# Optimization experiments

Hardware: AMD Instinct MI355X
Metric: run time of the kernel (lower is better)

The kernel has to match this reference:

```python
import jax, jax.numpy as jnp
import numpy as np

D_MODEL = 1024
NUM_HEADS = 16
D_K = D_MODEL // NUM_HEADS


def setup_inputs() -> dict:
    key = jax.random.key(0)
    ks = jax.random.split(key, 11)
    B, S = 2, 2048
    scale = 1.0 / np.sqrt(D_MODEL)
    inp = {
        'q': jax.random.normal(ks[0], (B, S, D_MODEL), jnp.float32),
        'k': jax.random.normal(ks[1], (B, S, D_MODEL), jnp.float32),
        'v': jax.random.normal(ks[2], (B, S, D_MODEL), jnp.float32),
        'Wq': jax.random.normal(ks[3], (D_MODEL, D_MODEL), jnp.float32) * scale,
        'bq': jnp.zeros((D_MODEL,), jnp.float32),
        'Wk': jax.random.normal(ks[4], (D_MODEL, D_MODEL), jnp.float32) * scale,
        'bk': jnp.zeros((D_MODEL,), jnp.float32),
        'Wv': jax.random.normal(ks[5], (D_MODEL, D_MODEL), jnp.float32) * scale,
        'bv': jnp.zeros((D_MODEL,), jnp.float32),
        'Wo': jax.random.normal(ks[6], (D_MODEL, D_MODEL), jnp.float32) * scale,
        'bo': jnp.zeros((D_MODEL,), jnp.float32),
    }
    return inp


def _split_heads(x):
    # [B, S, d_model] -> [B, H, S, d_k]
    B, S, _ = x.shape
    return x.reshape(B, S, NUM_HEADS, D_K).transpose(0, 2, 1, 3)


def reference(q, k, v, Wq, bq, Wk, bk, Wv, bv, Wo, bo):
    B, S, _ = q.shape
    qh = _split_heads(q @ Wq + bq)
    kh = _split_heads(k @ Wk + bk)
    vh = _split_heads(v @ Wv + bv)
    scores = jnp.einsum('bhsd,bhtd->bhst', qh, kh) / np.sqrt(D_K)
    attn = jax.nn.softmax(scores, axis=-1)  # dropout is identity in eval
    out = jnp.einsum('bhst,bhtd->bhsd', attn, vh)
    out = out.transpose(0, 2, 1, 3).reshape(B, S, D_MODEL)
    return out @ Wo + bo
```

## Files before the change

kernel.cpp:

```cpp
#include <hip/hip_runtime.h>

typedef unsigned short u16;
typedef unsigned int u32;
typedef __attribute__((ext_vector_type(4))) float f32x4;
typedef __attribute__((ext_vector_type(16))) float f32x16;
typedef __attribute__((ext_vector_type(8))) short bf16x8;
typedef __attribute__((ext_vector_type(4))) unsigned short u16x4;
typedef __attribute__((ext_vector_type(8))) unsigned short u16x8;
typedef __attribute__((ext_vector_type(4))) unsigned int u32x4;

#define S_LEN 2048
#define DMODEL 1024

__device__ __forceinline__ float bf2f(u16 u) {
  union { unsigned int i; float f; } c; c.i = ((unsigned int)u) << 16; return c.f;
}
__device__ __forceinline__ u16 f2bf(float f) {
  union { float f; unsigned int i; } c; c.f = f;
  unsigned int v = c.i + 0x7FFFu + ((c.i >> 16) & 1u);
  return (u16)(v >> 16);
}
__device__ __forceinline__ u32 cvtpk(float lo, float hi) {
  u32 r;
  asm("v_cvt_pk_bf16_f32 %0, %1, %2" : "=v"(r) : "v"(lo), "v"(hi));
  return r;
}

typedef const __attribute__((address_space(1))) void gv_t;
typedef __attribute__((address_space(3))) void lv_t;
__device__ __forceinline__ void gload_lds16(const void* g, void* l) {
  __builtin_amdgcn_global_load_lds((gv_t*)g, (lv_t*)l, 16, 0, 0);
}

__global__ __launch_bounds__(256) void k_cvt(const float* __restrict__ src,
                                             u16* __restrict__ dst, int n8) {
  int i = blockIdx.x * 256 + threadIdx.x;
  if (i >= n8) return;
  f32x4 a = ((const f32x4*)src)[i * 2];
  f32x4 b = ((const f32x4*)src)[i * 2 + 1];
  u16x8 o;
#pragma unroll
  for (int j = 0; j < 4; ++j) { o[j] = f2bf(a[j]); o[j + 4] = f2bf(b[j]); }
  ((u16x8*)dst)[i] = o;
}

__global__ __launch_bounds__(256) void k_twcvt(const float* __restrict__ src,
                                               u16* __restrict__ dst, int R, int C) {
  __shared__ u16 tile[64][68];
  int tiles_c = C >> 6;
  int tr = blockIdx.x / tiles_c, tc = blockIdx.x - tr * tiles_c;
  int r0 = tr << 6, c0 = tc << 6;
  int t = threadIdx.x;
#pragma unroll
  for (int i = 0; i < 4; ++i) {
    int e = (t + i * 256) << 2;
    int rr = e >> 6, cc = e & 63;
    f32x4 v = *(const f32x4*)&src[(size_t)(r0 + rr) * C + (c0 + cc)];
#pragma unroll
    for (int j = 0; j < 4; ++j) tile[rr][cc + j] = f2bf(v[j]);
  }
  __syncthreads();
#pragma unroll
  for (int i = 0; i < 4; ++i) {
    int e = (t + i * 256) << 2;
    int rr = e >> 6, cc = e & 63;
    u16x4 v;
#pragma unroll
    for (int j = 0; j < 4; ++j) v[j] = tile[cc + j][rr];
    *(u16x4*)&dst[(size_t)(c0 + rr) * R + (r0 + cc)] = v;
  }
}

__global__ __launch_bounds__(256) void k_packK(const u16* __restrict__ Ck,
                                               u16* __restrict__ Kp) {
  int flat = blockIdx.x * 256 + threadIdx.x;
  int lane = flat & 63, kd = (flat >> 6) & 3, kt = (flat >> 8) & 63;
  int h = (flat >> 14) & 15, b = flat >> 18;
  int l31 = lane & 31, hi = lane >> 5;
  const u16* src = &Ck[(size_t)(b * 2048 + kt * 32 + l31) * 1024 + h * 64 + kd * 16 + hi * 8];
  ((u16x8*)Kp)[flat] = *(const u16x8*)src;
}

__global__ __launch_bounds__(256) void k_packV(const u16* __restrict__ Cv,
                                               u16* __restrict__ Vp) {
  int flat = blockIdx.x * 256 + threadIdx.x;
  int lane = flat & 63, ks = (flat >> 6) & 3, dvh = (flat >> 8) & 1;
  int kt = (flat >> 9) & 31, h = (flat >> 14) & 15, b = flat >> 18;
  int l31 = lane & 31, hi = lane >> 5;
  const u16* src = &Cv[(size_t)(b * 2048 + kt * 64 + ks * 16 + hi * 8) * 1024 + h * 64 + dvh * 32 + l31];
  u16x8 o;
#pragma unroll
  for (int j = 0; j < 8; ++j) o[j] = src[(size_t)j * 1024];
  ((u16x8*)Vp)[flat] = o;
}

struct GemmSet { const u16* A; const u16* Bt; const float* bias; void* C; };
struct GemmArgs { GemmSet s[3]; };

template <int OUTF32>
__global__ __launch_bounds__(256) void k_gemm_bt(GemmArgs ga) {
  constexpr int K = 1024, N = 1024;
  __shared__ __align__(16) u16 Al[128 * 32];
  __shared__ __align__(16) u16 Bl[128 * 32];
  int mat = blockIdx.x >> 8;
  int t = blockIdx.x & 255;
  int m0 = (t & 31) << 7;
  int n0 = (t >> 5) << 7;
  const u16* A = ga.s[mat].A;
  const u16* Bt = ga.s[mat].Bt;
  int lane = threadIdx.x & 63, w = threadIdx.x >> 6;
  int g = lane >> 4, cl = lane & 15;
  int wr = w >> 1, wc = w & 1;
  f32x4 zero4 = {0.f, 0.f, 0.f, 0.f};
  f32x4 acc[4][4];
#pragma unroll
  for (int i = 0; i < 4; ++i)
#pragma unroll
    for (int j = 0; j < 4; ++j) acc[i][j] = zero4;

  int srow0 = w * 32 + (lane >> 2);
  int scol = (lane & 3) << 3;
  for (int kt = 0; kt < K / 32; ++kt) {
    int k0 = kt << 5;
#pragma unroll
    for (int c = 0; c < 2; ++c) {
      int row = srow0 + c * 16;
      gload_lds16(&A[(size_t)(m0 + row) * K + k0 + scol], &Al[w * 1024 + c * 512]);
      gload_lds16(&Bt[(size_t)(n0 + row) * K + k0 + scol], &Bl[w * 1024 + c * 512]);
    }
    __syncthreads();
    bf16x8 af[4], bfm[4];
#pragma unroll
    for (int i = 0; i < 4; ++i) {
      af[i]  = *(const bf16x8*)&Al[(wr * 64 + i * 16 + cl) * 32 + g * 8];
      bfm[i] = *(const bf16x8*)&Bl[(wc * 64 + i * 16 + cl) * 32 + g * 8];
    }
#pragma unroll
    for (int mi = 0; mi < 4; ++mi)
#pragma unroll
      for (int ni = 0; ni < 4; ++ni)
        acc[mi][ni] = __builtin_amdgcn_mfma_f32_16x16x32_bf16(af[mi], bfm[ni], acc[mi][ni], 0, 0, 0);
    __syncthreads();
  }
  const float* bias = ga.s[mat].bias;
#pragma unroll
  for (int ni = 0; ni < 4; ++ni) {
    int n = n0 + wc * 64 + ni * 16 + cl;
    float bv = bias[n];
#pragma unroll
    for (int mi = 0; mi < 4; ++mi) {
      int r0 = m0 + wr * 64 + mi * 16 + g * 4;
#pragma unroll
      for (int r = 0; r < 4; ++r) {
        float val = acc[mi][ni][r] + bv;
        if (OUTF32) ((float*)ga.s[mat].C)[(size_t)(r0 + r) * N + n] = val;
        else        ((u16*)ga.s[mat].C)[(size_t)(r0 + r) * N + n] = f2bf(val);
      }
    }
  }
}

__global__ __launch_bounds__(256) void k_attn2(const u16* __restrict__ Q,
                                               const u16* __restrict__ Kp,
                                               const u16* __restrict__ Vp,
                                               u16* __restrict__ O) {
  int lane = threadIdx.x & 63, w = threadIdx.x >> 6;
  int l31 = lane & 31, hi = lane >> 5;
  int bx = blockIdx.x;
  int logical = (bx & 7) * 64 + (bx >> 3);
  int bh = logical >> 4, qt = logical & 15;
  int b = bh >> 4, h = bh & 15;
  const u16* Qb = Q + (size_t)b * S_LEN * DMODEL + h * 64;
  const u16* Kph = Kp + (size_t)(b * 16 + h) * (64 * 4 * 64 * 8);
  const u16* Vph = Vp + (size_t)(b * 16 + h) * (32 * 2 * 4 * 64 * 8);
  u16* Ob = O + (size_t)b * S_LEN * DMODEL + h * 64;
  int qbase = qt * 128 + w * 32;

  bf16x8 qf[4];
  const u16* qp = &Qb[(size_t)(qbase + l31) * DMODEL + hi * 8];
#pragma unroll
  for (int kd = 0; kd < 4; ++kd) qf[kd] = *(const bf16x8*)&qp[kd * 16];

  f32x16 zero16 = {0};
  f32x16 oa0 = zero16, oa1 = zero16;
  float m = -3.0e38f, lsum = 0.f;
  const float INVSQ = 0.125f;

  for (int kt = 0; kt < S_LEN / 64; ++kt) {
    const u16* kpt = Kph + (size_t)kt * 4096 + (size_t)lane * 8;
    const u16* vpt = Vph + (size_t)kt * 4096 + (size_t)lane * 8;
    bf16x8 vf0[4], vf1[4];
#pragma unroll
    for (int ks = 0; ks < 4; ++ks) {
      vf0[ks] = *(const bf16x8*)&vpt[ks * 512];
      vf1[ks] = *(const bf16x8*)&vpt[2048 + ks * 512];
    }
    f32x16 s0 = zero16, s1 = zero16;
#pragma unroll
    for (int kd = 0; kd < 4; ++kd) {
      bf16x8 kfa = *(const bf16x8*)&kpt[kd * 512];
      bf16x8 kfb = *(const bf16x8*)&kpt[2048 + kd * 512];
      s0 = __builtin_amdgcn_mfma_f32_32x32x16_bf16(kfa, qf[kd], s0, 0, 0, 0);
      s1 = __builtin_amdgcn_mfma_f32_32x32x16_bf16(kfb, qf[kd], s1, 0, 0, 0);
    }

    float t0 = fmaxf(s0[0], s0[1]), t1 = fmaxf(s0[2], s0[3]);
    float t2 = fmaxf(s0[4], s0[5]), t3 = fmaxf(s0[6], s0[7]);
#pragma unroll
    for (int r = 8; r < 16; r += 4) {
      t0 = fmaxf(t0, fmaxf(s0[r], s0[r + 1]));
      t1 = fmaxf(t1, fmaxf(s0[r + 2], s0[r + 3]));
    }
#pragma unroll
    for (int r = 0; r < 16; r += 4) {
      t2 = fmaxf(t2, fmaxf(s1[r], s1[r + 1]));
      t3 = fmaxf(t3, fmaxf(s1[r + 2], s1[r + 3]));
    }
    float tm = fmaxf(fmaxf(t0, t1), fmaxf(t2, t3));

    if (!__all(tm <= m + 64.0f)) {
      float tmf = fmaxf(tm, __shfl_xor(tm, 32, 64));
      float mnew = fmaxf(m, tmf);
      float alpha = __expf((m - mnew) * INVSQ);
#pragma unroll
      for (int r = 0; r < 16; ++r) {
        float ar = __shfl(alpha, ((r & 3) + 8 * (r >> 2)) + 4 * hi, 64);
        oa0[r] *= ar; oa1[r] *= ar;
      }
      lsum *= alpha;
      m = mnew;
    }

    float rs0 = 0.f, rs1 = 0.f;
#pragma unroll
    for (int r = 0; r < 16; ++r) {
      float p0 = __expf((s0[r] - m) * INVSQ);
      float p1 = __expf((s1[r] - m) * INVSQ);
      s0[r] = p0; s1[r] = p1;
      rs0 += p0; rs1 += p1;
    }
    float rs = rs0 + rs1;
    lsum += rs + __shfl_xor(rs, 32, 64);

    bf16x8 af[4];
    {
      u32 w0 = cvtpk(s0[0], s0[1]),  w1 = cvtpk(s0[2], s0[3]);
      u32 w2 = cvtpk(s0[4], s0[5]),  w3 = cvtpk(s0[6], s0[7]);
      u32 w4 = cvtpk(s0[8], s0[9]),  w5 = cvtpk(s0[10], s0[11]);
      u32 w6 = cvtpk(s0[12], s0[13]), w7 = cvtpk(s0[14], s0[15]);
      u32 x0 = __shfl_xor(w0, 32, 64), x1 = __shfl_xor(w1, 32, 64);
      u32 x2 = __shfl_xor(w2, 32, 64), x3 = __shfl_xor(w3, 32, 64);
      u32 x4 = __shfl_xor(w4, 32, 64), x5 = __shfl_xor(w5, 32, 64);
      u32 x6 = __shfl_xor(w6, 32, 64), x7 = __shfl_xor(w7, 32, 64);
      union { u32x4 u; bf16x8 v; } c0, c1;
      c0.u = u32x4{hi ? x2 : w0, hi ? x3 : w1, hi ? w2 : x0, hi ? w3 : x1};
      c1.u = u32x4{hi ? x6 : w4, hi ? x7 : w5, hi ? w6 : x4, hi ? w7 : x5};
      af[0] = c0.v; af[1] = c1.v;
    }
    {
      u32 w0 = cvtpk(s1[0], s1[1]),  w1 = cvtpk(s1[2], s1[3]);
      u32 w2 = cvtpk(s1[4], s1[5]),  w3 = cvtpk(s1[6], s1[7]);
      u32 w4 = cvtpk(s1[8], s1[9]),  w5 = cvtpk(s1[10], s1[11]);
      u32 w6 = cvtpk(s1[12], s1[13]), w7 = cvtpk(s1[14], s1[15]);
      u32 x0 = __shfl_xor(w0, 32, 64), x1 = __shfl_xor(w1, 32, 64);
      u32 x2 = __shfl_xor(w2, 32, 64), x3 = __shfl_xor(w3, 32, 64);
      u32 x4 = __shfl_xor(w4, 32, 64), x5 = __shfl_xor(w5, 32, 64);
      u32 x6 = __shfl_xor(w6, 32, 64), x7 = __shfl_xor(w7, 32, 64);
      union { u32x4 u; bf16x8 v; } c0, c1;
      c0.u = u32x4{hi ? x2 : w0, hi ? x3 : w1, hi ? w2 : x0, hi ? w3 : x1};
      c1.u = u32x4{hi ? x6 : w4, hi ? x7 : w5, hi ? w6 : x4, hi ? w7 : x5};
      af[2] = c0.v; af[3] = c1.v;
    }

#pragma unroll
    for (int ks = 0; ks < 4; ++ks) {
      oa0 = __builtin_amdgcn_mfma_f32_32x32x16_bf16(af[ks], vf0[ks], oa0, 0, 0, 0);
      oa1 = __builtin_amdgcn_mfma_f32_32x32x16_bf16(af[ks], vf1[ks], oa1, 0, 0, 0);
    }
  }

  float invl = 1.0f / lsum;
#pragma unroll
  for (int r = 0; r < 16; ++r) {
    float ir = __shfl(invl, ((r & 3) + 8 * (r >> 2)) + 4 * hi, 64);
    int row = qbase + ((r & 3) + 8 * (r >> 2)) + 4 * hi;
    Ob[(size_t)row * DMODEL + l31]      = f2bf(oa0[r] * ir);
    Ob[(size_t)row * DMODEL + 32 + l31] = f2bf(oa1[r] * ir);
  }
}

extern "C" void kernel_launch(void* const* d_in, const int* in_sizes, int n_in,
                              void* d_out, int out_size, void* d_ws, size_t ws_size,
                              hipStream_t stream) {
  const float* q  = (const float*)d_in[0];
  const float* k  = (const float*)d_in[1];
  const float* v  = (const float*)d_in[2];
  const float* Wq = (const float*)d_in[3];
  const float* bq = (const float*)d_in[4];
  const float* Wk = (const float*)d_in[5];
  const float* bk = (const float*)d_in[6];
  const float* Wv = (const float*)d_in[7];
  const float* bv = (const float*)d_in[8];
  const float* Wo = (const float*)d_in[9];
  const float* bo = (const float*)d_in[10];
  float* out = (float*)d_out;
  char* ws = (char*)d_ws;
  const size_t MB = 1024 * 1024;
  u16* wtq = (u16*)(ws + 0 * MB);
  u16* wtk = (u16*)(ws + 2 * MB);
  u16* wtv = (u16*)(ws + 4 * MB);
  u16* wto = (u16*)(ws + 6 * MB);
  u16* qb  = (u16*)(ws + 8 * MB);
  u16* kb  = (u16*)(ws + 16 * MB);
  u16* vb  = (u16*)(ws + 24 * MB);
  u16* Cq  = (u16*)(ws + 32 * MB);
  u16* Ck  = (u16*)(ws + 40 * MB);
  u16* Cv  = (u16*)(ws + 48 * MB);
  u16* Kp  = qb;
  u16* Vp  = vb;
  u16* O   = kb;

  const int NTOK = 2 * S_LEN * DMODEL;
  k_cvt<<<NTOK / 8 / 256, 256, 0, stream>>>(q, qb, NTOK / 8);
  k_cvt<<<NTOK / 8 / 256, 256, 0, stream>>>(k, kb, NTOK / 8);
  k_cvt<<<NTOK / 8 / 256, 256, 0, stream>>>(v, vb, NTOK / 8);

  k_twcvt<<<256, 256, 0, stream>>>(Wq, wtq, 1024, 1024);
  k_twcvt<<<256, 256, 0, stream>>>(Wk, wtk, 1024, 1024);
  k_twcvt<<<256, 256, 0, stream>>>(Wv, wtv, 1024, 1024);
  k_twcvt<<<256, 256, 0, stream>>>(Wo, wto, 1024, 1024);

  GemmArgs ga;
  ga.s[0] = {qb, wtq, bq, (void*)Cq};
  ga.s[1] = {kb, wtk, bk, (void*)Ck};
  ga.s[2] = {vb, wtv, bv, (void*)Cv};
  k_gemm_bt<0><<<768, 256, 0, stream>>>(ga);

  k_packK<<<2048, 256, 0, stream>>>(Ck, Kp);
  k_packV<<<2048, 256, 0, stream>>>(Cv, Vp);

  k_attn2<<<512, 256, 0, stream>>>(Cq, Kp, Vp, O);

  GemmArgs go;
  go.s[0] = {O, wto, bo, (void*)out};
  go.s[1] = go.s[0];
  go.s[2] = go.s[0];
  k_gemm_bt<1><<<256, 256, 0, stream>>>(go);
}
```

Before: 273.2 us.

## Split attention KV range across wave pairs and merge launches

The attention kernel now assigns 64 queries per block, with two wave pairs each covering half of the key sequence. The partial outputs, maxes and sums are merged through LDS with a flash-decoding style rescale. This doubles the block count to 1024 to improve occupancy and shortens each wave's serial loop. The conversion, weight-transpose and pack kernels are also fused into single launches to cut launch overhead, at the cost of extra LDS use and a block-level sync in attention.

```diff
diff --git a/kernel.cpp b/kernel.cpp
--- a/kernel.cpp
+++ b/kernel.cpp
@@ -12,9 +12,6 @@
 #define S_LEN 2048
 #define DMODEL 1024
 
-__device__ __forceinline__ float bf2f(u16 u) {
-  union { unsigned int i; float f; } c; c.i = ((unsigned int)u) << 16; return c.f;
-}
 __device__ __forceinline__ u16 f2bf(float f) {
   union { float f; unsigned int i; } c; c.f = f;
   unsigned int v = c.i + 0x7FFFu + ((c.i >> 16) & 1u);
@@ -32,23 +29,33 @@
   __builtin_amdgcn_global_load_lds((gv_t*)g, (lv_t*)l, 16, 0, 0);
 }
 
-__global__ __launch_bounds__(256) void k_cvt(const float* __restrict__ src,
-                                             u16* __restrict__ dst, int n8) {
+__global__ __launch_bounds__(256) void k_cvt3(const float* __restrict__ s0,
+                                              const float* __restrict__ s1,
+                                              const float* __restrict__ s2,
+                                              u16* __restrict__ d0,
+                                              u16* __restrict__ d1,
+                                              u16* __restrict__ d2) {
   int i = blockIdx.x * 256 + threadIdx.x;
-  if (i >= n8) return;
-  f32x4 a = ((const f32x4*)src)[i * 2];
-  f32x4 b = ((const f32x4*)src)[i * 2 + 1];
+  int seg = i >> 19, idx = i & 524287;
+  const float* s = seg == 0 ? s0 : (seg == 1 ? s1 : s2);
+  u16* d = seg == 0 ? d0 : (seg == 1 ? d1 : d2);
+  f32x4 a = ((const f32x4*)s)[idx * 2];
+  f32x4 b = ((const f32x4*)s)[idx * 2 + 1];
   u16x8 o;
 #pragma unroll
   for (int j = 0; j < 4; ++j) { o[j] = f2bf(a[j]); o[j + 4] = f2bf(b[j]); }
-  ((u16x8*)dst)[i] = o;
-}
-
-__global__ __launch_bounds__(256) void k_twcvt(const float* __restrict__ src,
-                                               u16* __restrict__ dst, int R, int C) {
+  ((u16x8*)d)[idx] = o;
+}
+
+struct TwArgs { const float* src[4]; u16* dst[4]; };
+__global__ __launch_bounds__(256) void k_twcvt4(TwArgs ta) {
   __shared__ u16 tile[64][68];
-  int tiles_c = C >> 6;
-  int tr = blockIdx.x / tiles_c, tc = blockIdx.x - tr * tiles_c;
+  int wsel = blockIdx.x >> 8;
+  int bx = blockIdx.x & 255;
+  const float* src = ta.src[wsel];
+  u16* dst = ta.dst[wsel];
+  const int R = 1024, C = 1024;
+  int tr = bx >> 4, tc = bx & 15;
   int r0 = tr << 6, c0 = tc << 6;
   int t = threadIdx.x;
 #pragma unroll
@@ -71,27 +78,29 @@
   }
 }
 
-__global__ __launch_bounds__(256) void k_packK(const u16* __restrict__ Ck,
-                                               u16* __restrict__ Kp) {
-  int flat = blockIdx.x * 256 + threadIdx.x;
-  int lane = flat & 63, kd = (flat >> 6) & 3, kt = (flat >> 8) & 63;
-  int h = (flat >> 14) & 15, b = flat >> 18;
-  int l31 = lane & 31, hi = lane >> 5;
-  const u16* src = &Ck[(size_t)(b * 2048 + kt * 32 + l31) * 1024 + h * 64 + kd * 16 + hi * 8];
-  ((u16x8*)Kp)[flat] = *(const u16x8*)src;
-}
-
-__global__ __launch_bounds__(256) void k_packV(const u16* __restrict__ Cv,
-                                               u16* __restrict__ Vp) {
-  int flat = blockIdx.x * 256 + threadIdx.x;
-  int lane = flat & 63, ks = (flat >> 6) & 3, dvh = (flat >> 8) & 1;
-  int kt = (flat >> 9) & 31, h = (flat >> 14) & 15, b = flat >> 18;
-  int l31 = lane & 31, hi = lane >> 5;
-  const u16* src = &Cv[(size_t)(b * 2048 + kt * 64 + ks * 16 + hi * 8) * 1024 + h * 64 + dvh * 32 + l31];
-  u16x8 o;
-#pragma unroll
-  for (int j = 0; j < 8; ++j) o[j] = src[(size_t)j * 1024];
-  ((u16x8*)Vp)[flat] = o;
+__global__ __launch_bounds__(256) void k_pack(const u16* __restrict__ Ck,
+                                              const u16* __restrict__ Cv,
+                                              u16* __restrict__ Kp,
+                                              u16* __restrict__ Vp) {
+  int bx = blockIdx.x;
+  if (bx < 2048) {
+    int flat = bx * 256 + threadIdx.x;
+    int lane = flat & 63, kd = (flat >> 6) & 3, kt = (flat >> 8) & 63;
+    int h = (flat >> 14) & 15, b = flat >> 18;
+    int l31 = lane & 31, hi = lane >> 5;
+    const u16* src = &Ck[(size_t)(b * 2048 + kt * 32 + l31) * 1024 + h * 64 + kd * 16 + hi * 8];
+    ((u16x8*)Kp)[flat] = *(const u16x8*)src;
+  } else {
+    int flat = (bx - 2048) * 256 + threadIdx.x;
+    int lane = flat & 63, ks = (flat >> 6) & 3, dvh = (flat >> 8) & 1;
+    int kt = (flat >> 9) & 31, h = (flat >> 14) & 15, b = flat >> 18;
+    int l31 = lane & 31, hi = lane >> 5;
+    const u16* src = &Cv[(size_t)(b * 2048 + kt * 64 + ks * 16 + hi * 8) * 1024 + h * 64 + dvh * 32 + l31];
+    u16x8 o;
+#pragma unroll
+    for (int j = 0; j < 8; ++j) o[j] = src[(size_t)j * 1024];
+    ((u16x8*)Vp)[flat] = o;
+  }
 }
 
 struct GemmSet { const u16* A; const u16* Bt; const float* bias; void* C; };
@@ -160,21 +169,24 @@
   }
 }
 
-__global__ __launch_bounds__(256) void k_attn2(const u16* __restrict__ Q,
+__global__ __launch_bounds__(256) void k_attn3(const u16* __restrict__ Q,
                                                const u16* __restrict__ Kp,
                                                const u16* __restrict__ Vp,
                                                u16* __restrict__ O) {
+  __shared__ __align__(16) float Ol[2][32][64];
+  __shared__ float Ml[2][32][2];
   int lane = threadIdx.x & 63, w = threadIdx.x >> 6;
   int l31 = lane & 31, hi = lane >> 5;
+  int half = w >> 1, sub = w & 1;
   int bx = blockIdx.x;
-  int logical = (bx & 7) * 64 + (bx >> 3);
-  int bh = logical >> 4, qt = logical & 15;
+  int logical = (bx & 7) * 128 + (bx >> 3);
+  int bh = logical >> 5, qblk = logical & 31;
   int b = bh >> 4, h = bh & 15;
   const u16* Qb = Q + (size_t)b * S_LEN * DMODEL + h * 64;
   const u16* Kph = Kp + (size_t)(b * 16 + h) * (64 * 4 * 64 * 8);
   const u16* Vph = Vp + (size_t)(b * 16 + h) * (32 * 2 * 4 * 64 * 8);
   u16* Ob = O + (size_t)b * S_LEN * DMODEL + h * 64;
-  int qbase = qt * 128 + w * 32;
+  int qbase = qblk * 64 + sub * 32;
 
   bf16x8 qf[4];
   const u16* qp = &Qb[(size_t)(qbase + l31) * DMODEL + hi * 8];
@@ -186,7 +198,8 @@
   float m = -3.0e38f, lsum = 0.f;
   const float INVSQ = 0.125f;
 
-  for (int kt = 0; kt < S_LEN / 64; ++kt) {
+  int kt0 = half * 16;
+  for (int kt = kt0; kt < kt0 + 16; ++kt) {
     const u16* kpt = Kph + (size_t)kt * 4096 + (size_t)lane * 8;
     const u16* vpt = Vph + (size_t)kt * 4096 + (size_t)lane * 8;
     bf16x8 vf0[4], vf1[4];
@@ -279,13 +292,34 @@
     }
   }
 
-  float invl = 1.0f / lsum;
-#pragma unroll
-  for (int r = 0; r < 16; ++r) {
-    float ir = __shfl(invl, ((r & 3) + 8 * (r >> 2)) + 4 * hi, 64);
-    int row = qbase + ((r & 3) + 8 * (r >> 2)) + 4 * hi;
-    Ob[(size_t)row * DMODEL + l31]      = f2bf(oa0[r] * ir);
-    Ob[(size_t)row * DMODEL + 32 + l31] = f2bf(oa1[r] * ir);
+  if (half == 1) {
+#pragma unroll
+    for (int r = 0; r < 16; ++r) {
+      int q = ((r & 3) + 8 * (r >> 2)) + 4 * hi;
+      Ol[sub][q][l31] = oa0[r];
+      Ol[sub][q][l31 + 32] = oa1[r];
+    }
+    if (hi == 0) { Ml[sub][l31][0] = m; Ml[sub][l31][1] = lsum; }
+  }
+  __syncthreads();
+  if (half == 0) {
+    float m1 = Ml[sub][l31][0], l1 = Ml[sub][l31][1];
+    float M = fmaxf(m, m1);
+    float a0 = __expf((m - M) * INVSQ);
+    float a1 = __expf((m1 - M) * INVSQ);
+    float invl = 1.0f / (a0 * lsum + a1 * l1);
+    float c0 = a0 * invl, c1 = a1 * invl;
+#pragma unroll
+    for (int r = 0; r < 16; ++r) {
+      int q = ((r & 3) + 8 * (r >> 2)) + 4 * hi;
+      float f0 = __shfl(c0, q, 64);
+      float f1 = __shfl(c1, q, 64);
+      int row = qbase + q;
+      float o0 = oa0[r] * f0 + Ol[sub][q][l31] * f1;
+      float o1 = oa1[r] * f0 + Ol[sub][q][l31 + 32] * f1;
+      Ob[(size_t)row * DMODEL + l31]      = f2bf(o0);
+      Ob[(size_t)row * DMODEL + 32 + l31] = f2bf(o1);
+    }
   }
 }
 
@@ -320,15 +354,12 @@
   u16* Vp  = vb;
   u16* O   = kb;
 
-  const int NTOK = 2 * S_LEN * DMODEL;
-  k_cvt<<<NTOK / 8 / 256, 256, 0, stream>>>(q, qb, NTOK / 8);
-  k_cvt<<<NTOK / 8 / 256, 256, 0, stream>>>(k, kb, NTOK / 8);
-  k_cvt<<<NTOK / 8 / 256, 256, 0, stream>>>(v, vb, NTOK / 8);
-
-  k_twcvt<<<256, 256, 0, stream>>>(Wq, wtq, 1024, 1024);
-  k_twcvt<<<256, 256, 0, stream>>>(Wk, wtk, 1024, 1024);
-  k_twcvt<<<256, 256, 0, stream>>>(Wv, wtv, 1024, 1024);
-  k_twcvt<<<256, 256, 0, stream>>>(Wo, wto, 1024, 1024);
+  k_cvt3<<<6144, 256, 0, stream>>>(q, k, v, qb, kb, vb);
+
+  TwArgs ta;
+  ta.src[0] = Wq; ta.src[1] = Wk; ta.src[2] = Wv; ta.src[3] = Wo;
+  ta.dst[0] = wtq; ta.dst[1] = wtk; ta.dst[2] = wtv; ta.dst[3] = wto;
+  k_twcvt4<<<1024, 256, 0, stream>>>(ta);
 
   GemmArgs ga;
   ga.s[0] = {qb, wtq, bq, (void*)Cq};
@@ -336,10 +367,9 @@
   ga.s[2] = {vb, wtv, bv, (void*)Cv};
   k_gemm_bt<0><<<768, 256, 0, stream>>>(ga);
 
-  k_packK<<<2048, 256, 0, stream>>>(Ck, Kp);
-  k_packV<<<2048, 256, 0, stream>>>(Cv, Vp);
-
-  k_attn2<<<512, 256, 0, stream>>>(Cq, Kp, Vp, O);
+  k_pack<<<4096, 256, 0, stream>>>(Ck, Cv, Kp, Vp);
+
+  k_attn3<<<1024, 256, 0, stream>>>(Cq, Kp, Vp, O);
 
   GemmArgs go;
   go.s[0] = {O, wto, bo, (void*)out};
```

New measurement: 261.8 us. -4.2%, faster.
